# Kernel tuning notes

Measured on AMD Instinct MI355X. Metric: run time of the kernel, lower is better.

Reference implementation:

```python
import jax, jax.numpy as jnp
import numpy as np

T = 2048      # num_tokens == max_seq_len
D = 4096      # d_in
H = 32        # num_heads
G = 8         # num_kv_groups
HD = 128      # head_dim
GS = H // G   # group_size = 4
EPS = 1e-6


def _make_rope(t, hd):
    inv_freq = 1.0 / (10000.0 ** (np.arange(0, hd, 2, dtype=np.float64) / hd))
    freqs = np.outer(np.arange(t, dtype=np.float64), inv_freq)      # [T, HD/2]
    emb = np.concatenate([freqs, freqs], axis=-1)                   # [T, HD]
    return (jnp.asarray(np.cos(emb), jnp.float32),
            jnp.asarray(np.sin(emb), jnp.float32))


def setup_inputs() -> dict:
    key = jax.random.key(0)
    ks = jax.random.split(key, 6)
    x = jax.random.normal(ks[0], (T, D), jnp.float32)
    # causal mask: True = masked (upper triangle above diagonal)
    mask = jnp.triu(jnp.ones((T, T), jnp.bool_), k=1)
    cos, sin = _make_rope(T, HD)
    s = 0.02
    Wq = jax.random.normal(ks[1], (D, H * HD), jnp.float32) * s
    Wk = jax.random.normal(ks[2], (D, G * HD), jnp.float32) * s
    Wv = jax.random.normal(ks[3], (D, G * HD), jnp.float32) * s
    Wo = jax.random.normal(ks[4], (H * HD, D), jnp.float32) * s
    qn_w = jnp.ones((HD,), jnp.float32)
    kn_w = jnp.ones((HD,), jnp.float32)
    return {"x": x, "mask": mask, "cos": cos, "sin": sin,
            "Wq": Wq, "Wk": Wk, "Wv": Wv, "Wo": Wo,
            "qn_w": qn_w, "kn_w": kn_w}


def _rmsnorm(u, w):
    # normalize over head_dim (last axis), eps inside sqrt
    var = jnp.mean(jnp.square(u), axis=-1, keepdims=True)
    return u * jax.lax.rsqrt(var + EPS) * w


def _rope(u, cos, sin):
    # rotate-half RoPE; u: [heads, T, HD], cos/sin: [T, HD]
    hd = u.shape[-1]
    u1, u2 = u[..., : hd // 2], u[..., hd // 2:]
    rot = jnp.concatenate([-u2, u1], axis=-1)
    return u * cos[None] + rot * sin[None]


def reference(x, mask, cos, sin, Wq, Wk, Wv, Wo, qn_w, kn_w):
    t = x.shape[0]
    q = (x @ Wq).reshape(t, H, HD).transpose(1, 0, 2)   # [H, T, HD]
    k = (x @ Wk).reshape(t, G, HD).transpose(1, 0, 2)   # [G, T, HD]
    v = (x @ Wv).reshape(t, G, HD).transpose(1, 0, 2)   # [G, T, HD]
    q = _rmsnorm(q, qn_w)
    k = _rmsnorm(k, kn_w)
    q = _rope(q, cos, sin)
    k = _rope(k, cos, sin)
    # GQA expansion: repeat_interleave along head axis
    k = jnp.repeat(k, GS, axis=0)                       # [H, T, HD]
    v = jnp.repeat(v, GS, axis=0)                       # [H, T, HD]
    scores = jnp.einsum('hqd,hkd->hqk', q, k) / (HD ** 0.5)
    scores = jnp.where(mask[None], -jnp.inf, scores)
    w = jax.nn.softmax(scores, axis=-1)
    attn = jnp.einsum('hqk,hkd->hqd', w, v)             # [H, T, HD]
    attn = attn.transpose(1, 0, 2).reshape(t, H * HD)
    return attn @ Wo
```

## Files before the change

### kernel.cpp

```cpp
#include <hip/hip_runtime.h>

#define T_ 2048
#define D_ 4096
#define H_ 32
#define G_ 8
#define HD_ 128

typedef float f32x4 __attribute__((ext_vector_type(4)));
typedef __bf16 bf16x8 __attribute__((ext_vector_type(8)));
typedef unsigned short u16x8 __attribute__((ext_vector_type(8)));
typedef unsigned short u16x4 __attribute__((ext_vector_type(4)));

__device__ __forceinline__ unsigned short f2bf(float f) {
  unsigned u = __builtin_bit_cast(unsigned, f);
  u += 0x7FFFu + ((u >> 16) & 1u);
  return (unsigned short)(u >> 16);
}
__device__ __forceinline__ float bf2f(unsigned short h) {
  return __builtin_bit_cast(float, (unsigned)h << 16);
}

__device__ __forceinline__ void gload_lds16(const unsigned short* g, unsigned short* l) {
  __builtin_amdgcn_global_load_lds((const __attribute__((address_space(1))) void*)g,
                                   (__attribute__((address_space(3))) void*)l, 16, 0, 0);
}

__global__ __launch_bounds__(256) void convert_bf16(const float* __restrict__ in,
                                                    unsigned short* __restrict__ out) {
  const size_t i = ((size_t)blockIdx.x * 256 + threadIdx.x) * 8;
  float4 a = *(const float4*)(in + i);
  float4 b = *(const float4*)(in + i + 4);
  u16x8 o;
  o[0] = f2bf(a.x); o[1] = f2bf(a.y); o[2] = f2bf(a.z); o[3] = f2bf(a.w);
  o[4] = f2bf(b.x); o[5] = f2bf(b.y); o[6] = f2bf(b.z); o[7] = f2bf(b.w);
  *(u16x8*)(out + i) = o;
}

__global__ __launch_bounds__(256) void add_halves(const float* __restrict__ p,
                                                  float* __restrict__ out) {
  const size_t half = (size_t)2048 * 4096;
  const size_t stride = (size_t)gridDim.x * 256 * 4;
  for (size_t i = ((size_t)blockIdx.x * 256 + threadIdx.x) * 4; i < half; i += stride) {
    float4 a = *(const float4*)(p + i);
    float4 b = *(const float4*)(p + half + i);
    a.x += b.x; a.y += b.y; a.z += b.z; a.w += b.w;
    *(float4*)(out + i) = a;
  }
}

__global__ __launch_bounds__(256) void transpose_convert(const float* __restrict__ Wm,
                                                         unsigned short* __restrict__ Wt,
                                                         int R, int C) {
  __shared__ float tile[64][65];
  const int r0 = blockIdx.x * 64, c0 = blockIdx.y * 64;
  const int lr4 = threadIdx.x >> 6, lc = threadIdx.x & 63;
#pragma unroll
  for (int i = 0; i < 16; ++i) {
    int r = i * 4 + lr4;
    tile[r][lc] = Wm[(size_t)(r0 + r) * C + c0 + lc];
  }
  __syncthreads();
#pragma unroll
  for (int i = 0; i < 16; ++i) {
    int r = i * 4 + lr4;
    Wt[(size_t)(c0 + r) * R + r0 + lc] = f2bf(tile[lc][r]);
  }
}

__global__ __launch_bounds__(256) void transpose_v(const unsigned short* __restrict__ v,
                                                   unsigned short* __restrict__ vt, int stride) {
  __shared__ unsigned short tile[64][65];
  const int t0 = blockIdx.x * 64, d0 = blockIdx.y * 64, g = blockIdx.z;
  const int lr4 = threadIdx.x >> 6, lc = threadIdx.x & 63;
#pragma unroll
  for (int i = 0; i < 16; ++i) {
    int r = i * 4 + lr4;
    tile[r][lc] = v[(size_t)(t0 + r) * stride + g * HD_ + d0 + lc];
  }
  __syncthreads();
#pragma unroll
  for (int i = 0; i < 16; ++i) {
    int r = i * 4 + lr4;
    vt[((size_t)g * HD_ + d0 + r) * T_ + t0 + lc] = tile[lc][r];
  }
}

__global__ __launch_bounds__(256) void norm_rope(const unsigned short* __restrict__ raw,
                                                 int stride,
                                                 unsigned short* __restrict__ outp,
                                                 const float* __restrict__ w,
                                                 const float* __restrict__ cs,
                                                 const float* __restrict__ sn, int NH) {
  const int row = blockIdx.x * 4 + (threadIdx.x >> 6);
  const int lane = threadIdx.x & 63;
  const int t = row / NH, h = row - t * NH;
  const unsigned short* src = raw + (size_t)t * stride + h * HD_;
  float u1 = bf2f(src[lane]);
  float u2 = bf2f(src[lane + 64]);
  float ss = u1 * u1 + u2 * u2;
#pragma unroll
  for (int m = 1; m < 64; m <<= 1) ss += __shfl_xor(ss, m);
  float rr = rsqrtf(ss * (1.f / 128.f) + 1e-6f);
  float c = cs[(size_t)t * HD_ + lane];
  float s = sn[(size_t)t * HD_ + lane];
  float a = u1 * rr * w[lane];
  float b = u2 * rr * w[lane + 64];
  unsigned short* dst = outp + ((size_t)h * T_ + t) * HD_;
  dst[lane]      = f2bf(a * c - b * s);
  dst[lane + 64] = f2bf(b * c + a * s);
}

template <int MQ, int NQ>
__device__ __forceinline__ void mfma_quad(f32x4 (&acc)[2][4][2][2], bf16x8 (&af)[4][2],
                                          bf16x8 (&BF)[2][2]) {
  __builtin_amdgcn_s_setprio(1);
#pragma unroll
  for (int fm = 0; fm < 4; ++fm)
#pragma unroll
    for (int fn = 0; fn < 2; ++fn) {
      f32x4 a = acc[MQ][fm][NQ][fn];
      a = __builtin_amdgcn_mfma_f32_16x16x32_bf16(af[fm][0], BF[fn][0], a, 0, 0, 0);
      a = __builtin_amdgcn_mfma_f32_16x16x32_bf16(af[fm][1], BF[fn][1], a, 0, 0, 0);
      acc[MQ][fm][NQ][fn] = a;
    }
  __builtin_amdgcn_s_setprio(0);
}

template <int OUTF32>
__global__ __launch_bounds__(512, 2) void gemm256(const unsigned short* __restrict__ A,
                                                  const unsigned short* __restrict__ Bt,
                                                  void* __restrict__ Cv, int M, int N,
                                                  int KLEN, int LDA) {
  __shared__ __align__(16) unsigned short lds[65536];
  const int tid = threadIdx.x;
  const int wid = tid >> 6, lane = tid & 63;
  const int lr = lane & 15, lhi = lane >> 4, lhi8 = lhi * 8;
  const int wr = wid >> 2, wcn = wid & 3;
  const int wr64 = wr * 64, wcn32 = wcn * 32;

  int flat = (blockIdx.z * gridDim.y + blockIdx.y) * gridDim.x + blockIdx.x;
  int nwg = gridDim.x * gridDim.y * gridDim.z;
  int swz = (flat & 7) * (nwg >> 3) + (flat >> 3);
  const int bx = swz & 7;
  const int rest = swz >> 3;
  const int by = rest % gridDim.y;
  const int kz = rest / gridDim.y;
  const int brow = bx * 256;
  const int bcol = by * 256;

  A += (size_t)kz * KLEN;
  Bt += (size_t)kz * KLEN;

  const int nt = KLEN >> 6;

  f32x4 acc[2][4][2][2];
#pragma unroll
  for (int a = 0; a < 2; ++a)
#pragma unroll
    for (int b = 0; b < 4; ++b)
#pragma unroll
      for (int c = 0; c < 2; ++c)
#pragma unroll
        for (int d = 0; d < 2; ++d) acc[a][b][c][d] = (f32x4){0.f, 0.f, 0.f, 0.f};

  const int sl8 = ((lane & 7) ^ (lane >> 3)) * 8;
  const size_t gA0 = (size_t)(brow + wid * 16 + (lane >> 3)) * LDA + sl8;
  const size_t gB0 = (size_t)(bcol + wid * 16 + (lane >> 3)) * LDA + sl8;
  const int ldst0 = wid * 1024;

  auto stageA = [&](int ddB, int half, int ktp) {
#pragma unroll
    for (int l = 0; l < 2; ++l)
      gload_lds16(A + gA0 + (size_t)(half * 128 + l * 8) * LDA + ktp * 64,
                  &lds[ddB + half * 8192 + ldst0 + l * 512]);
  };
  auto stageB = [&](int ddB, int half, int ktp) {
#pragma unroll
    for (int l = 0; l < 2; ++l)
      gload_lds16(Bt + gB0 + (size_t)(half * 128 + l * 8) * LDA + ktp * 64,
                  &lds[32768 + ddB + half * 8192 + ldst0 + l * 512]);
  };

  bf16x8 af[4][2], bf0[2][2], bf1[2][2];
  auto readA = [&](int dB, int mqOff) {
#pragma unroll
    for (int fm = 0; fm < 4; ++fm) {
      int row = wr64 + fm * 16 + lr;
      int sw = (row & 7) << 3;
      int base = dB + mqOff + row * 64;
      af[fm][0] = *(const bf16x8*)&lds[base + (lhi8 ^ sw)];
      af[fm][1] = *(const bf16x8*)&lds[base + ((32 + lhi8) ^ sw)];
    }
  };
  auto readB = [&](int dB, int nqOff, bf16x8 (&bf)[2][2]) {
#pragma unroll
    for (int fn = 0; fn < 2; ++fn) {
      int row = wcn32 + fn * 16 + lr;
      int sw = (row & 7) << 3;
      int base = 32768 + dB + nqOff + row * 64;
      bf[fn][0] = *(const bf16x8*)&lds[base + (lhi8 ^ sw)];
      bf[fn][1] = *(const bf16x8*)&lds[base + ((32 + lhi8) ^ sw)];
    }
  };

  stageA(0, 0, 0); stageA(0, 1, 0); stageB(0, 0, 0); stageB(0, 1, 0);
  stageA(16384, 0, 1); stageB(16384, 1, 1);
  asm volatile("s_waitcnt vmcnt(4)" ::: "memory");
  __builtin_amdgcn_s_barrier();

  for (int t = 0; t < nt; ++t) {
    const int dB = (t & 1) ? 16384 : 0;
    const int dN = 16384 - dB;
    readA(dB, 0);
    readB(dB, 0, bf0);
    if (t + 1 < nt) stageA(dN, 1, t + 1);
    __builtin_amdgcn_s_barrier();
    mfma_quad<0, 0>(acc, af, bf0);
    __builtin_amdgcn_s_barrier();
    readB(dB, 8192, bf1);
    if (t + 1 < nt) stageB(dN, 0, t + 1);
    __builtin_amdgcn_s_barrier();
    mfma_quad<0, 1>(acc, af, bf1);
    __builtin_amdgcn_s_barrier();
    readA(dB, 8192);
    if (t + 2 < nt) stageA(dB, 0, t + 2);
    __builtin_amdgcn_s_barrier();
    mfma_quad<1, 1>(acc, af, bf1);
    __builtin_amdgcn_s_barrier();
    if (t + 2 < nt) stageB(dB, 1, t + 2);
    __builtin_amdgcn_s_barrier();
    mfma_quad<1, 0>(acc, af, bf0);
    if (t < nt - 2) asm volatile("s_waitcnt vmcnt(4)" ::: "memory");
    else if (t == nt - 2) asm volatile("s_waitcnt vmcnt(0)" ::: "memory");
    __builtin_amdgcn_s_barrier();
  }

  float* Cf = (float*)Cv + (size_t)kz * M * N;
#pragma unroll
  for (int mq = 0; mq < 2; ++mq)
#pragma unroll
    for (int fm = 0; fm < 4; ++fm)
#pragma unroll
      for (int nq = 0; nq < 2; ++nq)
#pragma unroll
        for (int fn = 0; fn < 2; ++fn) {
          int col = bcol + nq * 128 + wcn32 + fn * 16 + lr;
#pragma unroll
          for (int r = 0; r < 4; ++r) {
            int row = brow + mq * 128 + wr64 + fm * 16 + lhi * 4 + r;
            if (OUTF32)
              Cf[(size_t)row * N + col] = acc[mq][fm][nq][fn][r];
            else
              ((unsigned short*)Cv)[(size_t)row * N + col] = f2bf(acc[mq][fm][nq][fn][r]);
          }
        }
}

__global__ __launch_bounds__(512) void flash_attn(const unsigned short* __restrict__ q,
                                                  const unsigned short* __restrict__ k,
                                                  const unsigned short* __restrict__ vt,
                                                  unsigned short* __restrict__ attnb) {
  const int pairIdx = blockIdx.y;
  const int g = pairIdx >> 1;
  const int qc = gridDim.x - 1 - blockIdx.x;
  const int tid = threadIdx.x;
  const int wid = tid >> 6;
  const int lane = tid & 63;
  const int lr = lane & 15, lhi = lane >> 4;
  const int h = pairIdx * 2 + (wid >> 2);
  const int q0 = qc * 64 + (wid & 3) * 16;

  __shared__ __align__(16) unsigned short Ks[2][64 * HD_];
  __shared__ __align__(16) unsigned short Vs[2][HD_ * 64];
  __shared__ __align__(16) unsigned short p_lds_all[8][16 * 64];
  unsigned short* p_lds = p_lds_all[wid];

  const unsigned short* kg = k + (size_t)g * T_ * HD_;
  const unsigned short* vg = vt + (size_t)g * HD_ * T_;

  int ko[2], vo[2];
#pragma unroll
  for (int p = 0; p < 2; ++p) {
    int ob = (p * 512 + tid) * 16;
    int krow = ob >> 8, kb = ob & 255;
    ko[p] = krow * HD_ + ((kb ^ ((krow & 7) << 4)) >> 1);
    int vrow = ob >> 7, vb2 = ob & 127;
    vo[p] = vrow * T_ + ((vb2 ^ ((vrow & 7) << 4)) >> 1);
  }
  const int lbase = wid * 512;

  const int sx = (lr & 7) << 4;
  const float scale2 = 0.08838834764831845f * 1.4426950408889634f;

  bf16x8 qf[4];
  {
    const unsigned short* qrow = q + ((size_t)h * T_ + q0 + lr) * HD_ + lhi * 8;
#pragma unroll
    for (int c = 0; c < 4; ++c) qf[c] = *(const bf16x8*)(qrow + c * 32);
  }
  f32x4 accO[8];
#pragma unroll
  for (int i = 0; i < 8; ++i) accO[i] = (f32x4){0.f, 0.f, 0.f, 0.f};
  float mrow = -3e38f;
  float lrow = 0.f;

  const int ntile = qc + 1;

#pragma unroll
  for (int p = 0; p < 2; ++p) {
    gload_lds16(kg + ko[p], &Ks[0][p * 4096 + lbase]);
    gload_lds16(vg + vo[p], &Vs[0][p * 4096 + lbase]);
  }
  __syncthreads();

  for (int kt = 0; kt < ntile; ++kt) {
    const int b = kt & 1;
    const int kv0 = kt << 6;
    if (kt + 1 < ntile) {
      const size_t kofs = (size_t)(kv0 + 64) * HD_;
#pragma unroll
      for (int p = 0; p < 2; ++p) {
        gload_lds16(kg + kofs + ko[p], &Ks[b ^ 1][p * 4096 + lbase]);
        gload_lds16(vg + (kv0 + 64) + vo[p], &Vs[b ^ 1][p * 4096 + lbase]);
      }
    }
    f32x4 st[4];
    __builtin_amdgcn_s_setprio(1);
#pragma unroll
    for (int j = 0; j < 4; ++j) {
      st[j] = (f32x4){0.f, 0.f, 0.f, 0.f};
      const int krow = j * 16 + lr;
#pragma unroll
      for (int c = 0; c < 4; ++c) {
        bf16x8 kf = *(const bf16x8*)&Ks[b][krow * HD_ + (((c * 64 + lhi * 16) ^ sx) >> 1)];
        st[j] = __builtin_amdgcn_mfma_f32_16x16x32_bf16(kf, qf[c], st[j], 0, 0, 0);
      }
    }
    __builtin_amdgcn_s_setprio(0);
    if (kt == ntile - 1) {
#pragma unroll
      for (int j = 0; j < 4; ++j)
#pragma unroll
        for (int r = 0; r < 4; ++r)
          st[j][r] = (kv0 + j * 16 + lhi * 4 + r <= q0 + lr) ? st[j][r] * scale2 : -3e38f;
    } else {
#pragma unroll
      for (int j = 0; j < 4; ++j)
#pragma unroll
        for (int r = 0; r < 4; ++r) st[j][r] *= scale2;
    }
    float pm = st[0][0];
#pragma unroll
    for (int j = 0; j < 4; ++j)
#pragma unroll
      for (int r = 0; r < 4; ++r) pm = fmaxf(pm, st[j][r]);
    pm = fmaxf(pm, __shfl_xor(pm, 16));
    pm = fmaxf(pm, __shfl_xor(pm, 32));
    if (!__all(pm - mrow <= 8.f)) {
      float mnew = fmaxf(mrow, pm);
      float al = __builtin_amdgcn_exp2f(mrow - mnew);
      mrow = mnew;
      lrow *= al;
      float a0 = __shfl(al, lhi * 4 + 0);
      float a1 = __shfl(al, lhi * 4 + 1);
      float a2 = __shfl(al, lhi * 4 + 2);
      float a3 = __shfl(al, lhi * 4 + 3);
#pragma unroll
      for (int dt = 0; dt < 8; ++dt) {
        accO[dt][0] *= a0; accO[dt][1] *= a1; accO[dt][2] *= a2; accO[dt][3] *= a3;
      }
    }
    float ps = 0.f;
#pragma unroll
    for (int j = 0; j < 4; ++j)
#pragma unroll
      for (int r = 0; r < 4; ++r) {
        float e = __builtin_amdgcn_exp2f(st[j][r] - mrow);
        st[j][r] = e;
        ps += e;
      }
    ps += __shfl_xor(ps, 16);
    ps += __shfl_xor(ps, 32);
    lrow += ps;
#pragma unroll
    for (int j = 0; j < 4; ++j) {
      u16x4 pw;
      pw[0] = f2bf(st[j][0]); pw[1] = f2bf(st[j][1]);
      pw[2] = f2bf(st[j][2]); pw[3] = f2bf(st[j][3]);
      *(u16x4*)&p_lds[lr * 64 + (((j * 32 + lhi * 8) ^ sx) >> 1)] = pw;
    }
    bf16x8 pa0 = *(const bf16x8*)&p_lds[lr * 64 + (((lhi * 16) ^ sx) >> 1)];
    bf16x8 pa1 = *(const bf16x8*)&p_lds[lr * 64 + (((64 + lhi * 16) ^ sx) >> 1)];
    __builtin_amdgcn_s_setprio(1);
#pragma unroll
    for (int dt = 0; dt < 8; ++dt) {
      const int vrow = dt * 16 + lr;
      bf16x8 vf0 = *(const bf16x8*)&Vs[b][vrow * 64 + (((lhi * 16) ^ sx) >> 1)];
      bf16x8 vf1 = *(const bf16x8*)&Vs[b][vrow * 64 + (((64 + lhi * 16) ^ sx) >> 1)];
      accO[dt] = __builtin_amdgcn_mfma_f32_16x16x32_bf16(pa0, vf0, accO[dt], 0, 0, 0);
      accO[dt] = __builtin_amdgcn_mfma_f32_16x16x32_bf16(pa1, vf1, accO[dt], 0, 0, 0);
    }
    __builtin_amdgcn_s_setprio(0);
    __syncthreads();
  }
  float rinv = 1.f / lrow;
  float i0 = __shfl(rinv, lhi * 4 + 0);
  float i1 = __shfl(rinv, lhi * 4 + 1);
  float i2 = __shfl(rinv, lhi * 4 + 2);
  float i3 = __shfl(rinv, lhi * 4 + 3);
  float iv[4] = {i0, i1, i2, i3};
#pragma unroll
  for (int r = 0; r < 4; ++r) {
    size_t rowoff = (size_t)(q0 + lhi * 4 + r) * (H_ * HD_) + h * HD_;
#pragma unroll
    for (int dt = 0; dt < 8; ++dt) attnb[rowoff + dt * 16 + lr] = f2bf(accO[dt][r] * iv[r]);
  }
}

extern "C" void kernel_launch(void* const* d_in, const int* in_sizes, int n_in,
                              void* d_out, int out_size, void* d_ws, size_t ws_size,
                              hipStream_t stream) {
  const float* x = (const float*)d_in[0];
  const float* cosT = (const float*)d_in[2];
  const float* sinT = (const float*)d_in[3];
  const float* Wq = (const float*)d_in[4];
  const float* Wk = (const float*)d_in[5];
  const float* Wv = (const float*)d_in[6];
  const float* Wo = (const float*)d_in[7];
  const float* qn = (const float*)d_in[8];
  const float* kn = (const float*)d_in[9];

  unsigned char* w = (unsigned char*)d_ws;
  unsigned short* xb     = (unsigned short*)(w);
  unsigned short* WqkvT  = (unsigned short*)(w + 16777216);
  unsigned short* qkvraw = (unsigned short*)(w + 67108864);
  unsigned short* qbuf   = (unsigned short*)(w + 92274688);
  unsigned short* kbuf   = (unsigned short*)(w + 109051904);
  unsigned short* vtb    = (unsigned short*)(w + 113246208);
  unsigned short* WoT    = WqkvT;
  unsigned short* attnb  = xb;
  float* p0 = (float*)(w + 50331648);

  convert_bf16<<<dim3(4096), dim3(256), 0, stream>>>(x, xb);
  transpose_convert<<<dim3(64, 64), dim3(256), 0, stream>>>(Wq, WqkvT, 4096, 4096);
  transpose_convert<<<dim3(64, 16), dim3(256), 0, stream>>>(Wk, WqkvT + (size_t)4096 * 4096, 4096, 1024);
  transpose_convert<<<dim3(64, 16), dim3(256), 0, stream>>>(Wv, WqkvT + (size_t)5120 * 4096, 4096, 1024);

  gemm256<0><<<dim3(8, 24, 1), dim3(512), 0, stream>>>(xb, WqkvT, (void*)qkvraw, 2048, 6144, 4096, 4096);

  norm_rope<<<dim3(16384), dim3(256), 0, stream>>>(qkvraw, 6144, qbuf, qn, cosT, sinT, H_);
  norm_rope<<<dim3(4096), dim3(256), 0, stream>>>(qkvraw + 4096, 6144, kbuf, kn, cosT, sinT, G_);
  transpose_v<<<dim3(32, 2, 8), dim3(256), 0, stream>>>(qkvraw + 5120, vtb, 6144);
  transpose_convert<<<dim3(64, 64), dim3(256), 0, stream>>>(Wo, WoT, 4096, 4096);

  flash_attn<<<dim3(32, 16), dim3(512), 0, stream>>>(qbuf, kbuf, vtb, attnb);

  gemm256<1><<<dim3(8, 16, 2), dim3(512), 0, stream>>>(attnb, WoT, (void*)p0, 2048, 4096, 2048, 4096);
  add_halves<<<dim3(2048), dim3(256), 0, stream>>>(p0, (float*)d_out);
}
```

Before: 370.7 us.

## Retile GEMMs to 256xN blocks and drop split-K with its reduction kernel

Replaces the 256x256 GEMM kernel with a templated 256x(NF*64) kernel. The QKV projection now uses 256x192 tiles (8x32=256 blocks) and the output projection uses 256x128 tiles over the full K, which removes the split-K partial buffer and the add_halves reduction pass. The goal is better wave balance across the 256 CUs, fewer launches and less extra fp32 memory traffic. In exchange each block reuses less data per tile and runs a longer K loop, and the staging pipeline is restructured in a way that needs careful vmcnt bookkeeping.

```diff
diff --git a/kernel.cpp b/kernel.cpp
--- a/kernel.cpp
+++ b/kernel.cpp
@@ -34,18 +34,6 @@
   o[0] = f2bf(a.x); o[1] = f2bf(a.y); o[2] = f2bf(a.z); o[3] = f2bf(a.w);
   o[4] = f2bf(b.x); o[5] = f2bf(b.y); o[6] = f2bf(b.z); o[7] = f2bf(b.w);
   *(u16x8*)(out + i) = o;
-}
-
-__global__ __launch_bounds__(256) void add_halves(const float* __restrict__ p,
-                                                  float* __restrict__ out) {
-  const size_t half = (size_t)2048 * 4096;
-  const size_t stride = (size_t)gridDim.x * 256 * 4;
-  for (size_t i = ((size_t)blockIdx.x * 256 + threadIdx.x) * 4; i < half; i += stride) {
-    float4 a = *(const float4*)(p + i);
-    float4 b = *(const float4*)(p + half + i);
-    a.x += b.x; a.y += b.y; a.z += b.z; a.w += b.w;
-    *(float4*)(out + i) = a;
-  }
 }
 
 __global__ __launch_bounds__(256) void transpose_convert(const float* __restrict__ Wm,
@@ -110,150 +98,144 @@
   dst[lane + 64] = f2bf(b * c + a * s);
 }
 
-template <int MQ, int NQ>
-__device__ __forceinline__ void mfma_quad(f32x4 (&acc)[2][4][2][2], bf16x8 (&af)[4][2],
-                                          bf16x8 (&BF)[2][2]) {
+template <int NF, int MQ, int F0, int F1>
+__device__ __forceinline__ void mfma_g(f32x4 (&acc)[2][4][NF], bf16x8 (&af)[4][2],
+                                       bf16x8 (&bf)[NF][2]) {
   __builtin_amdgcn_s_setprio(1);
 #pragma unroll
   for (int fm = 0; fm < 4; ++fm)
 #pragma unroll
-    for (int fn = 0; fn < 2; ++fn) {
-      f32x4 a = acc[MQ][fm][NQ][fn];
-      a = __builtin_amdgcn_mfma_f32_16x16x32_bf16(af[fm][0], BF[fn][0], a, 0, 0, 0);
-      a = __builtin_amdgcn_mfma_f32_16x16x32_bf16(af[fm][1], BF[fn][1], a, 0, 0, 0);
-      acc[MQ][fm][NQ][fn] = a;
+    for (int fn = F0; fn < F1; ++fn) {
+      f32x4 a = acc[MQ][fm][fn];
+      a = __builtin_amdgcn_mfma_f32_16x16x32_bf16(af[fm][0], bf[fn][0], a, 0, 0, 0);
+      a = __builtin_amdgcn_mfma_f32_16x16x32_bf16(af[fm][1], bf[fn][1], a, 0, 0, 0);
+      acc[MQ][fm][fn] = a;
     }
   __builtin_amdgcn_s_setprio(0);
 }
 
-template <int OUTF32>
-__global__ __launch_bounds__(512, 2) void gemm256(const unsigned short* __restrict__ A,
-                                                  const unsigned short* __restrict__ Bt,
-                                                  void* __restrict__ Cv, int M, int N,
-                                                  int KLEN, int LDA) {
-  __shared__ __align__(16) unsigned short lds[65536];
+template <int NF, int OUTF32>
+__global__ __launch_bounds__(512, 2) void gemm2(const unsigned short* __restrict__ A,
+                                                const unsigned short* __restrict__ Bt,
+                                                void* __restrict__ Cv, int M, int N,
+                                                int K, int LDA) {
+  constexpr int BN = NF * 64;
+  constexpr int BBUF = NF * 4096;
+  __shared__ __align__(16) unsigned short lds[32768 + 2 * BBUF];
   const int tid = threadIdx.x;
   const int wid = tid >> 6, lane = tid & 63;
-  const int lr = lane & 15, lhi = lane >> 4, lhi8 = lhi * 8;
+  const int lr = lane & 15, lhi = lane >> 4;
   const int wr = wid >> 2, wcn = wid & 3;
-  const int wr64 = wr * 64, wcn32 = wcn * 32;
-
-  int flat = (blockIdx.z * gridDim.y + blockIdx.y) * gridDim.x + blockIdx.x;
-  int nwg = gridDim.x * gridDim.y * gridDim.z;
+  const int wr64 = wr * 64;
+
+  int flat = blockIdx.y * gridDim.x + blockIdx.x;
+  int nwg = gridDim.x * gridDim.y;
   int swz = (flat & 7) * (nwg >> 3) + (flat >> 3);
-  const int bx = swz & 7;
-  const int rest = swz >> 3;
-  const int by = rest % gridDim.y;
-  const int kz = rest / gridDim.y;
-  const int brow = bx * 256;
-  const int bcol = by * 256;
-
-  A += (size_t)kz * KLEN;
-  Bt += (size_t)kz * KLEN;
-
-  const int nt = KLEN >> 6;
-
-  f32x4 acc[2][4][2][2];
+  const int brow = (swz & 7) * 256;
+  const int bcol = (swz >> 3) * BN;
+
+  const int nt = K >> 6;
+
+  f32x4 acc[2][4][NF];
 #pragma unroll
   for (int a = 0; a < 2; ++a)
 #pragma unroll
     for (int b = 0; b < 4; ++b)
 #pragma unroll
-      for (int c = 0; c < 2; ++c)
-#pragma unroll
-        for (int d = 0; d < 2; ++d) acc[a][b][c][d] = (f32x4){0.f, 0.f, 0.f, 0.f};
-
-  const int sl8 = ((lane & 7) ^ (lane >> 3)) * 8;
-  const size_t gA0 = (size_t)(brow + wid * 16 + (lane >> 3)) * LDA + sl8;
-  const size_t gB0 = (size_t)(bcol + wid * 16 + (lane >> 3)) * LDA + sl8;
-  const int ldst0 = wid * 1024;
-
-  auto stageA = [&](int ddB, int half, int ktp) {
-#pragma unroll
-    for (int l = 0; l < 2; ++l)
-      gload_lds16(A + gA0 + (size_t)(half * 128 + l * 8) * LDA + ktp * 64,
-                  &lds[ddB + half * 8192 + ldst0 + l * 512]);
+      for (int c = 0; c < NF; ++c) acc[a][b][c] = (f32x4){0.f, 0.f, 0.f, 0.f};
+
+  const int t8 = tid >> 3;
+  const int srcCol = ((tid & 7) ^ (t8 & 7)) * 8;
+  auto stageA = [&](int d, int u, int ktp) {
+    gload_lds16(A + (size_t)(brow + u * 64 + t8) * LDA + ktp * 64 + srcCol,
+                &lds[d * 16384 + u * 4096 + tid * 8]);
   };
-  auto stageB = [&](int ddB, int half, int ktp) {
-#pragma unroll
-    for (int l = 0; l < 2; ++l)
-      gload_lds16(Bt + gB0 + (size_t)(half * 128 + l * 8) * LDA + ktp * 64,
-                  &lds[32768 + ddB + half * 8192 + ldst0 + l * 512]);
+  auto stageB = [&](int d, int v, int ktp) {
+    gload_lds16(Bt + (size_t)(bcol + v * 64 + t8) * LDA + ktp * 64 + srcCol,
+                &lds[32768 + d * BBUF + v * 4096 + tid * 8]);
   };
 
-  bf16x8 af[4][2], bf0[2][2], bf1[2][2];
-  auto readA = [&](int dB, int mqOff) {
+  bf16x8 af[4][2], bf[NF][2];
+  auto readA = [&](int d, int mq) {
 #pragma unroll
     for (int fm = 0; fm < 4; ++fm) {
-      int row = wr64 + fm * 16 + lr;
+      int row = mq * 128 + wr64 + fm * 16 + lr;
+      int base = d * 16384 + row * 64;
       int sw = (row & 7) << 3;
-      int base = dB + mqOff + row * 64;
-      af[fm][0] = *(const bf16x8*)&lds[base + (lhi8 ^ sw)];
-      af[fm][1] = *(const bf16x8*)&lds[base + ((32 + lhi8) ^ sw)];
+      af[fm][0] = *(const bf16x8*)&lds[base + ((lhi * 8) ^ sw)];
+      af[fm][1] = *(const bf16x8*)&lds[base + ((32 + lhi * 8) ^ sw)];
     }
   };
-  auto readB = [&](int dB, int nqOff, bf16x8 (&bf)[2][2]) {
-#pragma unroll
-    for (int fn = 0; fn < 2; ++fn) {
-      int row = wcn32 + fn * 16 + lr;
-      int sw = (row & 7) << 3;
-      int base = 32768 + dB + nqOff + row * 64;
-      bf[fn][0] = *(const bf16x8*)&lds[base + (lhi8 ^ sw)];
-      bf[fn][1] = *(const bf16x8*)&lds[base + ((32 + lhi8) ^ sw)];
-    }
+  auto readBf = [&](int d, int fn, bf16x8 (&slot)[2]) {
+    int row = wcn * (16 * NF) + fn * 16 + lr;
+    int base = 32768 + d * BBUF + row * 64;
+    int sw = (row & 7) << 3;
+    slot[0] = *(const bf16x8*)&lds[base + ((lhi * 8) ^ sw)];
+    slot[1] = *(const bf16x8*)&lds[base + ((32 + lhi * 8) ^ sw)];
   };
 
-  stageA(0, 0, 0); stageA(0, 1, 0); stageB(0, 0, 0); stageB(0, 1, 0);
-  stageA(16384, 0, 1); stageB(16384, 1, 1);
-  asm volatile("s_waitcnt vmcnt(4)" ::: "memory");
+  stageA(0, 0, 0); stageA(0, 1, 0); stageA(0, 2, 0); stageA(0, 3, 0);
+#pragma unroll
+  for (int v = 0; v < NF; ++v) stageB(0, v, 0);
+  stageA(1, 0, 1); stageA(1, 1, 1);
+  asm volatile("s_waitcnt vmcnt(2)" ::: "memory");
   __builtin_amdgcn_s_barrier();
 
   for (int t = 0; t < nt; ++t) {
-    const int dB = (t & 1) ? 16384 : 0;
-    const int dN = 16384 - dB;
-    readA(dB, 0);
-    readB(dB, 0, bf0);
-    if (t + 1 < nt) stageA(dN, 1, t + 1);
-    __builtin_amdgcn_s_barrier();
-    mfma_quad<0, 0>(acc, af, bf0);
-    __builtin_amdgcn_s_barrier();
-    readB(dB, 8192, bf1);
-    if (t + 1 < nt) stageB(dN, 0, t + 1);
-    __builtin_amdgcn_s_barrier();
-    mfma_quad<0, 1>(acc, af, bf1);
-    __builtin_amdgcn_s_barrier();
-    readA(dB, 8192);
-    if (t + 2 < nt) stageA(dB, 0, t + 2);
-    __builtin_amdgcn_s_barrier();
-    mfma_quad<1, 1>(acc, af, bf1);
-    __builtin_amdgcn_s_barrier();
-    if (t + 2 < nt) stageB(dB, 1, t + 2);
-    __builtin_amdgcn_s_barrier();
-    mfma_quad<1, 0>(acc, af, bf0);
-    if (t < nt - 2) asm volatile("s_waitcnt vmcnt(4)" ::: "memory");
-    else if (t == nt - 2) asm volatile("s_waitcnt vmcnt(0)" ::: "memory");
-    __builtin_amdgcn_s_barrier();
-  }
-
-  float* Cf = (float*)Cv + (size_t)kz * M * N;
+    const int d = t & 1, dn = d ^ 1;
+    if constexpr (NF == 2) {
+      readA(d, 0); readBf(d, 0, bf[0]); readBf(d, 1, bf[1]);
+      if (t + 1 < nt) { stageA(dn, 2, t + 1); stageA(dn, 3, t + 1);
+                        stageB(dn, 0, t + 1); stageB(dn, 1, t + 1); }
+      __builtin_amdgcn_s_barrier();
+      mfma_g<NF, 0, 0, 2>(acc, af, bf);
+      __builtin_amdgcn_s_barrier();
+      readA(d, 1);
+      if (t + 2 < nt) { stageA(d, 0, t + 2); stageA(d, 1, t + 2); }
+      __builtin_amdgcn_s_barrier();
+      mfma_g<NF, 1, 0, 2>(acc, af, bf);
+      if (t < nt - 2) asm volatile("s_waitcnt vmcnt(2)" ::: "memory");
+      else if (t == nt - 2) asm volatile("s_waitcnt vmcnt(0)" ::: "memory");
+      __builtin_amdgcn_s_barrier();
+    } else {
+      readA(d, 0); readBf(d, 0, bf[0]); readBf(d, 1, bf[1]);
+      if (t + 1 < nt) { stageA(dn, 2, t + 1); stageA(dn, 3, t + 1); }
+      __builtin_amdgcn_s_barrier();
+      mfma_g<NF, 0, 0, 2>(acc, af, bf);
+      __builtin_amdgcn_s_barrier();
+      readBf(d, 2, bf[2]);
+      if (t + 1 < nt) { stageB(dn, 0, t + 1); stageB(dn, 1, t + 1); stageB(dn, 2, t + 1); }
+      __builtin_amdgcn_s_barrier();
+      mfma_g<NF, 0, 2, 3>(acc, af, bf);
+      __builtin_amdgcn_s_barrier();
+      readA(d, 1);
+      if (t + 2 < nt) { stageA(d, 0, t + 2); stageA(d, 1, t + 2); }
+      __builtin_amdgcn_s_barrier();
+      mfma_g<NF, 1, 0, 2>(acc, af, bf);
+      __builtin_amdgcn_s_barrier();
+      mfma_g<NF, 1, 2, 3>(acc, af, bf);
+      if (t < nt - 2) asm volatile("s_waitcnt vmcnt(2)" ::: "memory");
+      else if (t == nt - 2) asm volatile("s_waitcnt vmcnt(0)" ::: "memory");
+      __builtin_amdgcn_s_barrier();
+    }
+  }
+
 #pragma unroll
   for (int mq = 0; mq < 2; ++mq)
 #pragma unroll
     for (int fm = 0; fm < 4; ++fm)
 #pragma unroll
-      for (int nq = 0; nq < 2; ++nq)
-#pragma unroll
-        for (int fn = 0; fn < 2; ++fn) {
-          int col = bcol + nq * 128 + wcn32 + fn * 16 + lr;
-#pragma unroll
-          for (int r = 0; r < 4; ++r) {
-            int row = brow + mq * 128 + wr64 + fm * 16 + lhi * 4 + r;
-            if (OUTF32)
-              Cf[(size_t)row * N + col] = acc[mq][fm][nq][fn][r];
-            else
-              ((unsigned short*)Cv)[(size_t)row * N + col] = f2bf(acc[mq][fm][nq][fn][r]);
-          }
+      for (int fn = 0; fn < NF; ++fn) {
+        int col = bcol + wcn * (16 * NF) + fn * 16 + lr;
+#pragma unroll
+        for (int r = 0; r < 4; ++r) {
+          int row = brow + mq * 128 + wr64 + fm * 16 + lhi * 4 + r;
+          if (OUTF32)
+            ((float*)Cv)[(size_t)row * N + col] = acc[mq][fm][fn][r];
+          else
+            ((unsigned short*)Cv)[(size_t)row * N + col] = f2bf(acc[mq][fm][fn][r]);
         }
+      }
 }
 
 __global__ __launch_bounds__(512) void flash_attn(const unsigned short* __restrict__ q,
@@ -439,14 +421,13 @@
   unsigned short* vtb    = (unsigned short*)(w + 113246208);
   unsigned short* WoT    = WqkvT;
   unsigned short* attnb  = xb;
-  float* p0 = (float*)(w + 50331648);
 
   convert_bf16<<<dim3(4096), dim3(256), 0, stream>>>(x, xb);
   transpose_convert<<<dim3(64, 64), dim3(256), 0, stream>>>(Wq, WqkvT, 4096, 4096);
   transpose_convert<<<dim3(64, 16), dim3(256), 0, stream>>>(Wk, WqkvT + (size_t)4096 * 4096, 4096, 1024);
   transpose_convert<<<dim3(64, 16), dim3(256), 0, stream>>>(Wv, WqkvT + (size_t)5120 * 4096, 4096, 1024);
 
-  gemm256<0><<<dim3(8, 24, 1), dim3(512), 0, stream>>>(xb, WqkvT, (void*)qkvraw, 2048, 6144, 4096, 4096);
+  gemm2<3, 0><<<dim3(8, 32), dim3(512), 0, stream>>>(xb, WqkvT, (void*)qkvraw, 2048, 6144, 4096, 4096);
 
   norm_rope<<<dim3(16384), dim3(256), 0, stream>>>(qkvraw, 6144, qbuf, qn, cosT, sinT, H_);
   norm_rope<<<dim3(4096), dim3(256), 0, stream>>>(qkvraw + 4096, 6144, kbuf, kn, cosT, sinT, G_);
@@ -455,6 +436,5 @@
 
   flash_attn<<<dim3(32, 16), dim3(512), 0, stream>>>(qbuf, kbuf, vtb, attnb);
 
-  gemm256<1><<<dim3(8, 16, 2), dim3(512), 0, stream>>>(attnb, WoT, (void*)p0, 2048, 4096, 2048, 4096);
-  add_halves<<<dim3(2048), dim3(256), 0, stream>>>(p0, (float*)d_out);
-}
+  gemm2<2, 1><<<dim3(8, 32), dim3(512), 0, stream>>>(attnb, WoT, d_out, 2048, 4096, 4096, 4096);
+}
```

Measured after the change: 350.2 us. -5.5%, faster.
